# Performance work log

Hardware: AMD Instinct MI355X
Metric: run time of the kernel (lower is better)

The kernel has to match this reference:

```python
import jax, jax.numpy as jnp
import numpy as np

N = 100000          # nodes
E = 1600000         # edges (avg degree 16)
IN_DIM = 64
HID = 64
OUT = 32
NUM_GRAPHS = 64


def setup_inputs() -> dict:
    key = jax.random.key(0)
    ks = jax.random.split(key, 12)
    x = jax.random.normal(ks[0], (N, IN_DIM), dtype=jnp.float32)
    edge_index = jax.random.randint(ks[1], (2, E), 0, N, dtype=jnp.int64)
    batch = jnp.sort(jax.random.randint(ks[2], (N,), 0, NUM_GRAPHS, dtype=jnp.int64))
    s = 0.05
    return {
        "x": x,
        "edge_index": edge_index,
        "batch": batch,
        "w1_init": jax.random.normal(ks[3], (IN_DIM, HID), dtype=jnp.float32) * s,
        "w1_root": jax.random.normal(ks[4], (IN_DIM, HID), dtype=jnp.float32) * s,
        "b1": jnp.zeros((HID,), dtype=jnp.float32),
        "w2_init": jax.random.normal(ks[5], (HID, HID), dtype=jnp.float32) * s,
        "w2_root": jax.random.normal(ks[6], (HID, HID), dtype=jnp.float32) * s,
        "b2": jnp.zeros((HID,), dtype=jnp.float32),
        "fc_w": jax.random.normal(ks[7], (HID, OUT), dtype=jnp.float32) * s,
        "fc_b": jnp.zeros((OUT,), dtype=jnp.float32),
    }


def reference(x, edge_index, batch, w1_init, w1_root, b1, w2_init, w2_root, b2, fc_w, fc_b):
    row, col = edge_index[0], edge_index[1]
    # gcn_norm without self loops (ARMAConv default): deg over target nodes
    ones_e = jnp.ones((E,), dtype=x.dtype)
    deg = jax.ops.segment_sum(ones_e, col, num_segments=N)
    dinv = jnp.where(deg > 0, jax.lax.rsqrt(jnp.maximum(deg, 1.0)), 0.0)
    norm = dinv[row] * dinv[col]  # [E]

    def propagate(h):  # out[col] += norm * h[row]
        return jax.ops.segment_sum(h[row] * norm[:, None], col, num_segments=N)

    # ARMAConv (K=1, T=1, act=None): A_hat (x W_init) + x W_root + b
    h = jax.nn.relu(propagate(x @ w1_init) + x @ w1_root + b1)
    h = jax.nn.relu(propagate(h @ w2_init) + h @ w2_root + b2)

    # global mean pool over graphs
    cnt = jax.ops.segment_sum(jnp.ones((N,), dtype=h.dtype), batch, num_segments=NUM_GRAPHS)
    pooled = jax.ops.segment_sum(h, batch, num_segments=NUM_GRAPHS) / jnp.maximum(cnt, 1.0)[:, None]

    return pooled @ fc_w + fc_b  # [NUM_GRAPHS, OUT]
```

## Files before the change

### kernel.cpp

```cpp
#include <hip/hip_runtime.h>
#include <hip/hip_bf16.h>


#define NB 256
#define CAP 5120
#define MAXB 400
#define P1_CHUNK 2048

typedef unsigned int uint32;
typedef unsigned short ushort16;
typedef __attribute__((ext_vector_type(8))) short short8;
typedef __attribute__((ext_vector_type(4))) float f32x4;

__device__ inline uint32 bf16rn(float f) {
    uint32 u = __float_as_uint(f);
    uint32 r = ((u >> 16) & 1u) + 0x7FFFu;
    return (u + r) >> 16;
}
__device__ inline uint32 pack_bf16(float a, float b) {
    return bf16rn(a) | (bf16rn(b) << 16);
}
__device__ inline float bflo(uint32 u) { return __uint_as_float(u << 16); }
__device__ inline float bfhi(uint32 u) { return __uint_as_float(u & 0xFFFF0000u); }

__global__ __launch_bounds__(256) void bucket_kernel(
    const int* __restrict__ row, const int* __restrict__ col,
    uint32* __restrict__ bpack, int* __restrict__ bcnt, int E,
    const float* __restrict__ W1i, const float* __restrict__ W1r,
    const float* __restrict__ W2i, const float* __restrict__ W2r,
    ushort16* __restrict__ wt) {
    __shared__ int hist[MAXB];
    __shared__ int ofs[MAXB];
    __shared__ int cur[MAXB];
    __shared__ int gbase[MAXB];
    __shared__ int s[256];
    __shared__ uint32 stage[P1_CHUNK];
    __shared__ unsigned short stage_bk[P1_CHUNK];

    int t = threadIdx.x;

    if (blockIdx.x < 128) {
        int idx = blockIdx.x * 256 + t;
        int m = idx >> 12;
        int r = idx & 4095;
        int d = r >> 6, k = r & 63;
        const float* W = (m < 2) ? W1i : (m < 4) ? W1r : (m < 6) ? W2i : W2r;
        float v = W[k * 64 + d];
        uint32 hi = bf16rn(v);
        uint32 outv;
        if (m & 1) {
            float hf = __uint_as_float(hi << 16);
            outv = bf16rn(v - hf);
        } else {
            outv = hi;
        }
        wt[(size_t)m * 4096 + d * 64 + k] = (unsigned short)outv;
        return;
    }

    for (int i = t; i < MAXB; i += 256) hist[i] = 0;
    __syncthreads();

    int e0 = (blockIdx.x - 128) * P1_CHUNK;
    int cntE = min(E - e0, P1_CHUNK);

    for (int i = t; i < cntE; i += 256) {
        int c = col[e0 + i];
        atomicAdd(&hist[c >> 8], 1);
    }
    __syncthreads();

    int i2 = 2 * t;
    int a = (i2 < MAXB) ? hist[i2] : 0;
    int b = (i2 + 1 < MAXB) ? hist[i2 + 1] : 0;
    s[t] = a + b;
    __syncthreads();
    for (int off = 1; off < 256; off <<= 1) {
        int x = (t >= off) ? s[t - off] : 0;
        __syncthreads();
        s[t] += x;
        __syncthreads();
    }
    int excl = (t > 0) ? s[t - 1] : 0;
    if (i2 < MAXB) ofs[i2] = excl;
    if (i2 + 1 < MAXB) ofs[i2 + 1] = excl + a;
    __syncthreads();

    for (int i = t; i < MAXB; i += 256) {
        cur[i] = ofs[i];
        gbase[i] = hist[i] ? atomicAdd(&bcnt[i], hist[i]) : 0;
    }
    __syncthreads();

    for (int i = t; i < cntE; i += 256) {
        int c = col[e0 + i];
        int r = row[e0 + i];
        int bk = c >> 8;
        int k = atomicAdd(&cur[bk], 1);
        stage[k] = ((uint32)(c & 255) << 24) | (uint32)r;
        stage_bk[k] = (unsigned short)bk;
    }
    __syncthreads();

    for (int i = t; i < cntE; i += 256) {
        uint32 pk = stage[i];
        int bk = stage_bk[i];
        int gd = gbase[bk] + (i - ofs[bk]);
        if (gd < CAP) bpack[(size_t)bk * CAP + gd] = pk;
    }
}

__global__ __launch_bounds__(1024) void csr_kernel(
    const uint32* __restrict__ bpack, const int* __restrict__ bcnt,
    int* __restrict__ es, int* __restrict__ nstart, int* __restrict__ ndeg,
    float* __restrict__ dinv, int n) {
    __shared__ uint32 sbp[CAP];
    __shared__ int h[NB];
    __shared__ int s[NB];
    __shared__ int cur[NB];
    int b = blockIdx.x, t = threadIdx.x;
    if (t < NB) h[t] = 0;
    __syncthreads();
    int cnt = min(bcnt[b], CAP);
    size_t base = (size_t)b * CAP;
    for (int i = t; i < cnt; i += 1024) {
        uint32 pk = bpack[base + i];
        sbp[i] = pk;
        atomicAdd(&h[pk >> 24], 1);
    }
    __syncthreads();
    if (t < NB) s[t] = h[t];
    __syncthreads();
    for (int off = 1; off < NB; off <<= 1) {
        int x = 0;
        if (t < NB && t >= off) x = s[t - off];
        __syncthreads();
        if (t < NB) s[t] += x;
        __syncthreads();
    }
    if (t < NB) {
        int myofs = s[t] - h[t];
        cur[t] = myofs;
        int node = b * NB + t;
        if (node < n) {
            nstart[node] = (int)base + myofs;
            ndeg[node] = h[t];
            dinv[node] = h[t] ? rsqrtf((float)h[t]) : 0.0f;
        }
    }
    __syncthreads();
    for (int i = t; i < cnt; i += 1024) {
        uint32 pk = sbp[i];
        int cl = (int)(pk >> 24);
        int p = atomicAdd(&cur[cl], 1);
        es[base + p] = (int)(pk & 0xFFFFFFu);
    }
}

__global__ __launch_bounds__(256) void gemm_mfma(
    const void* __restrict__ Xin,
    const ushort16* __restrict__ wt4,
    const float* __restrict__ bias, const float* __restrict__ dinv,
    ushort16* __restrict__ Ts, ushort16* __restrict__ Rs, int n, int xf32) {
    __shared__ unsigned short sXs[64 * 72];
    int t = threadIdx.x;
    int node0 = blockIdx.x * 64;

    if (xf32) {
        const float* X = (const float*)Xin;
        for (int i = t; i < 1024; i += 256) {
            int r = i >> 4, c4 = (i & 15) * 4;
            int node = node0 + r;
            float4 v = make_float4(0.f, 0.f, 0.f, 0.f);
            if (node < n) v = *(const float4*)&X[(size_t)node * 64 + c4];
            *(uint32*)&sXs[r * 72 + c4] = pack_bf16(v.x, v.y);
            *(uint32*)&sXs[r * 72 + c4 + 2] = pack_bf16(v.z, v.w);
        }
    } else {
        const uint32* Xb2 = (const uint32*)Xin;
        for (int i = t; i < 512; i += 256) {
            int r = i >> 3, kg = i & 7;
            int node = node0 + r;
            uint4 v = make_uint4(0u, 0u, 0u, 0u);
            if (node < n) v = *(const uint4*)&Xb2[(size_t)node * 32 + kg * 4];
            *(uint4*)&sXs[r * 72 + kg * 8] = v;
        }
    }

    int w = t >> 6;
    int lane = t & 63;
    int q = lane >> 4;
    int col = lane & 15;
    int dim = w * 16 + col;

    short8 bih[2], bil[2], brh[2], brl[2];
#pragma unroll
    for (int kh = 0; kh < 2; ++kh) {
        size_t o = (size_t)dim * 64 + kh * 32 + q * 8;
        bih[kh] = *(const short8*)&wt4[0 * 4096 + o];
        bil[kh] = *(const short8*)&wt4[1 * 4096 + o];
        brh[kh] = *(const short8*)&wt4[2 * 4096 + o];
        brl[kh] = *(const short8*)&wt4[3 * 4096 + o];
    }
    float4 bias4 = *(const float4*)&bias[w * 16 + q * 4];
    __syncthreads();

    unsigned short* TsU = (unsigned short*)Ts;
    unsigned short* RsU = (unsigned short*)Rs;

#pragma unroll
    for (int mt = 0; mt < 4; ++mt) {
        int rbase = mt * 16 + col;
        short8 a0 = *(const short8*)&sXs[rbase * 72 + q * 8];
        short8 a1 = *(const short8*)&sXs[rbase * 72 + 32 + q * 8];
        f32x4 accT = {0.f, 0.f, 0.f, 0.f};
        f32x4 accR = {0.f, 0.f, 0.f, 0.f};
        accT = __builtin_amdgcn_mfma_f32_16x16x32_bf16(bih[0], a0, accT, 0, 0, 0);
        accT = __builtin_amdgcn_mfma_f32_16x16x32_bf16(bih[1], a1, accT, 0, 0, 0);
        accT = __builtin_amdgcn_mfma_f32_16x16x32_bf16(bil[0], a0, accT, 0, 0, 0);
        accT = __builtin_amdgcn_mfma_f32_16x16x32_bf16(bil[1], a1, accT, 0, 0, 0);
        accR = __builtin_amdgcn_mfma_f32_16x16x32_bf16(brh[0], a0, accR, 0, 0, 0);
        accR = __builtin_amdgcn_mfma_f32_16x16x32_bf16(brh[1], a1, accR, 0, 0, 0);
        accR = __builtin_amdgcn_mfma_f32_16x16x32_bf16(brl[0], a0, accR, 0, 0, 0);
        accR = __builtin_amdgcn_mfma_f32_16x16x32_bf16(brl[1], a1, accR, 0, 0, 0);

        int node = node0 + mt * 16 + col;
        if (node < n) {
            float dv = dinv[node];
            uint2 pT, pR;
            pT.x = pack_bf16(accT[0] * dv, accT[1] * dv);
            pT.y = pack_bf16(accT[2] * dv, accT[3] * dv);
            pR.x = pack_bf16(accR[0] + bias4.x, accR[1] + bias4.y);
            pR.y = pack_bf16(accR[2] + bias4.z, accR[3] + bias4.w);
            size_t o = (size_t)node * 64 + w * 16 + q * 4;
            *(uint2*)&TsU[o] = pT;
            *(uint2*)&RsU[o] = pR;
        }
    }
}

__global__ __launch_bounds__(256) void gather_fused(
    const uint2* __restrict__ Ts2, const uint2* __restrict__ Rs2,
    const int* __restrict__ es, const int* __restrict__ nstart,
    const int* __restrict__ ndeg, const float* __restrict__ dinv,
    uint2* __restrict__ Hb2, int n) {
    int c = blockIdx.x * 4 + (threadIdx.x >> 6);
    if (c >= n) return;
    int lane = threadIdx.x & 63;
    int q = lane >> 4;
    int d4 = lane & 15;
    int deg = ndeg[c];
    int s0 = nstart[c];
    float a0 = 0.f, a1 = 0.f, a2 = 0.f, a3 = 0.f;
    for (int base = 0; base < deg; base += 64) {
        int m = min(deg - base, 64);
        int sid = (lane < m) ? __builtin_nontemporal_load(&es[s0 + base + lane]) : 0;
        for (int j = 0; j < m; j += 16) {
            int e0 = j + q, e1 = j + 4 + q, e2 = j + 8 + q, e3 = j + 12 + q;
            int r0 = __shfl(sid, e0);
            int r1 = __shfl(sid, e1);
            int r2 = __shfl(sid, e2);
            int r3 = __shfl(sid, e3);
            uint2 z = make_uint2(0u, 0u);
            uint2 v0 = (e0 < m) ? Ts2[(size_t)r0 * 16 + d4] : z;
            uint2 v1 = (e1 < m) ? Ts2[(size_t)r1 * 16 + d4] : z;
            uint2 v2 = (e2 < m) ? Ts2[(size_t)r2 * 16 + d4] : z;
            uint2 v3 = (e3 < m) ? Ts2[(size_t)r3 * 16 + d4] : z;
            a0 += bflo(v0.x) + bflo(v1.x) + bflo(v2.x) + bflo(v3.x);
            a1 += bfhi(v0.x) + bfhi(v1.x) + bfhi(v2.x) + bfhi(v3.x);
            a2 += bflo(v0.y) + bflo(v1.y) + bflo(v2.y) + bflo(v3.y);
            a3 += bfhi(v0.y) + bfhi(v1.y) + bfhi(v2.y) + bfhi(v3.y);
        }
    }
    a0 += __shfl_xor(a0, 16); a0 += __shfl_xor(a0, 32);
    a1 += __shfl_xor(a1, 16); a1 += __shfl_xor(a1, 32);
    a2 += __shfl_xor(a2, 16); a2 += __shfl_xor(a2, 32);
    a3 += __shfl_xor(a3, 16); a3 += __shfl_xor(a3, 32);
    if (lane < 16) {
        float dc = dinv[c];
        uint2 ur = Rs2[(size_t)c * 16 + d4];
        float h0 = fmaxf(fmaf(dc, a0, bflo(ur.x)), 0.0f);
        float h1 = fmaxf(fmaf(dc, a1, bfhi(ur.x)), 0.0f);
        float h2 = fmaxf(fmaf(dc, a2, bflo(ur.y)), 0.0f);
        float h3 = fmaxf(fmaf(dc, a3, bfhi(ur.y)), 0.0f);
        Hb2[(size_t)c * 16 + d4] = make_uint2(pack_bf16(h0, h1), pack_bf16(h2, h3));
    }
}

__global__ __launch_bounds__(256) void pool_kernel(
    const uint32* __restrict__ Hb, const int* __restrict__ batch,
    float* __restrict__ pooled, float* __restrict__ cnt, int n) {
    __shared__ float sAcc[64 * 64];
    __shared__ float sCnt[64];
    int tid = threadIdx.x;
    for (int i = tid; i < 4096; i += 256) sAcc[i] = 0.0f;
    if (tid < 64) sCnt[tid] = 0.0f;
    __syncthreads();

    int w = tid >> 6, lane = tid & 63;
    int half = lane >> 5, d2 = lane & 31;
    int s = blockIdx.x * 256 + w * 64;
    int e = min(s + 64, n);
    float a0 = 0.0f, a1 = 0.0f, c = 0.0f;
    int gcur = -1;
    for (int i = s + half; i < e; i += 2) {
        int g = batch[i];
        if (g != gcur) {
            if (gcur >= 0) {
                atomicAdd(&sAcc[gcur * 64 + 2 * d2], a0);
                atomicAdd(&sAcc[gcur * 64 + 2 * d2 + 1], a1);
                if (d2 == 0) atomicAdd(&sCnt[gcur], c);
            }
            gcur = g; a0 = 0.0f; a1 = 0.0f; c = 0.0f;
        }
        uint32 u = Hb[(size_t)i * 32 + d2];
        a0 += bflo(u);
        a1 += bfhi(u);
        c += 1.0f;
    }
    if (gcur >= 0) {
        atomicAdd(&sAcc[gcur * 64 + 2 * d2], a0);
        atomicAdd(&sAcc[gcur * 64 + 2 * d2 + 1], a1);
        if (d2 == 0) atomicAdd(&sCnt[gcur], c);
    }
    __syncthreads();
    for (int i = tid; i < 4096; i += 256) {
        float v = sAcc[i];
        if (v != 0.0f) atomicAdd(&pooled[i], v);
    }
    if (tid < 64) {
        float v = sCnt[tid];
        if (v != 0.0f) atomicAdd(&cnt[tid], v);
    }
}

__global__ void final_fc(const float* __restrict__ pooled, const float* __restrict__ cnt,
                         const float* __restrict__ fcw, const float* __restrict__ fcb,
                         float* __restrict__ out) {
    int idx = blockIdx.x * 256 + threadIdx.x;
    if (idx >= 64 * 32) return;
    int g = idx >> 5, o = idx & 31;
    float c = fmaxf(cnt[g], 1.0f);
    float acc = 0.0f;
#pragma unroll
    for (int k = 0; k < 64; ++k) acc = fmaf(pooled[g * 64 + k], fcw[k * 32 + o], acc);
    out[idx] = acc / c + fcb[o];
}

extern "C" void kernel_launch(void* const* d_in, const int* in_sizes, int n_in,
                              void* d_out, int out_size, void* d_ws, size_t ws_size,
                              hipStream_t stream) {
    const float* x       = (const float*)d_in[0];
    const int*   eidx    = (const int*)d_in[1];
    const int*   batch   = (const int*)d_in[2];
    const float* w1_init = (const float*)d_in[3];
    const float* w1_root = (const float*)d_in[4];
    const float* b1      = (const float*)d_in[5];
    const float* w2_init = (const float*)d_in[6];
    const float* w2_root = (const float*)d_in[7];
    const float* b2      = (const float*)d_in[8];
    const float* fc_w    = (const float*)d_in[9];
    const float* fc_b    = (const float*)d_in[10];
    float* out = (float*)d_out;

    const int N = in_sizes[0] / 64;
    const int E = in_sizes[1] / 2;
    const int* row = eidx;
    const int* col = eidx + E;

    const int B = (N + NB - 1) / NB;

    uint32* bpack = (uint32*)d_ws;
    int*   es     = (int*)(bpack + (size_t)B * CAP);
    int*   bcnt   = es + (size_t)B * CAP;
    float* pooled = (float*)(bcnt + MAXB);
    float* cnt    = pooled + 64 * 64;
    int*   nstart = (int*)(cnt + 64);
    int*   ndeg   = nstart + N;
    float* dinv   = (float*)(ndeg + N);
    uint32* wtU   = (uint32*)(dinv + N);
    uint32* Ts    = wtU + 16384;
    uint32* Rs    = Ts + (size_t)N * 32;
    uint32* Hb    = Rs + (size_t)N * 32;
    ushort16* wt  = (ushort16*)wtU;

    hipMemsetAsync(bcnt, 0, (size_t)(MAXB + 64 * 64 + 64) * sizeof(int), stream);

    const int EB = (E + P1_CHUNK - 1) / P1_CHUNK;
    bucket_kernel<<<128 + EB, 256, 0, stream>>>(row, col, bpack, bcnt, E,
                                                w1_init, w1_root, w2_init, w2_root, wt);
    csr_kernel<<<B, 1024, 0, stream>>>(bpack, bcnt, es, nstart, ndeg, dinv, N);

    gemm_mfma<<<(N + 63) / 64, 256, 0, stream>>>(x, wt, b1, dinv,
                                                 (ushort16*)Ts, (ushort16*)Rs, N, 1);
    gather_fused<<<(N + 3) / 4, 256, 0, stream>>>((const uint2*)Ts, (const uint2*)Rs,
                                                  es, nstart, ndeg, dinv, (uint2*)Hb, N);

    gemm_mfma<<<(N + 63) / 64, 256, 0, stream>>>(Hb, wt + (size_t)4 * 4096, b2, dinv,
                                                 (ushort16*)Ts, (ushort16*)Rs, N, 0);
    gather_fused<<<(N + 3) / 4, 256, 0, stream>>>((const uint2*)Ts, (const uint2*)Rs,
                                                  es, nstart, ndeg, dinv, (uint2*)Hb, N);

    pool_kernel<<<(N + 255) / 256, 256, 0, stream>>>(Hb, batch, pooled, cnt, N);
    final_fc<<<(64 * 32 + 255) / 256, 256, 0, stream>>>(pooled, cnt, fc_w, fc_b, out);
}
```

Baseline: 294.5 us.

## Replace bucketed CSR build with global-atomic degree count, scan, and scatter

Replaces the two-pass bucket/local-sort CSR construction with three simpler kernels: per-node degree counting via global atomics, a single-block prefix scan that also computes dinv, and an atomic scatter of row indices into the CSR edge array. This drops the fixed per-bucket capacity and the intermediate packed buffer. In exchange it uses 1.6M contended global atomics twice and a single-block serial scan over 100k nodes. Neighbor order within each node is no longer deterministic. The gather also drops its nontemporal load of edge sources.

```diff
diff --git a/kernel.cpp b/kernel.cpp
--- a/kernel.cpp
+++ b/kernel.cpp
@@ -3,9 +3,6 @@
 
 
 #define NB 256
-#define CAP 5120
-#define MAXB 400
-#define P1_CHUNK 2048
 
 typedef unsigned int uint32;
 typedef unsigned short ushort16;
@@ -23,20 +20,11 @@
 __device__ inline float bflo(uint32 u) { return __uint_as_float(u << 16); }
 __device__ inline float bfhi(uint32 u) { return __uint_as_float(u & 0xFFFF0000u); }
 
-__global__ __launch_bounds__(256) void bucket_kernel(
-    const int* __restrict__ row, const int* __restrict__ col,
-    uint32* __restrict__ bpack, int* __restrict__ bcnt, int E,
+__global__ __launch_bounds__(256) void deg_kernel(
+    const int* __restrict__ col, int* __restrict__ ndeg, int E,
     const float* __restrict__ W1i, const float* __restrict__ W1r,
     const float* __restrict__ W2i, const float* __restrict__ W2r,
     ushort16* __restrict__ wt) {
-    __shared__ int hist[MAXB];
-    __shared__ int ofs[MAXB];
-    __shared__ int cur[MAXB];
-    __shared__ int gbase[MAXB];
-    __shared__ int s[256];
-    __shared__ uint32 stage[P1_CHUNK];
-    __shared__ unsigned short stage_bk[P1_CHUNK];
-
     int t = threadIdx.x;
 
     if (blockIdx.x < 128) {
@@ -58,102 +46,76 @@
         return;
     }
 
-    for (int i = t; i < MAXB; i += 256) hist[i] = 0;
-    __syncthreads();
-
-    int e0 = (blockIdx.x - 128) * P1_CHUNK;
-    int cntE = min(E - e0, P1_CHUNK);
-
-    for (int i = t; i < cntE; i += 256) {
-        int c = col[e0 + i];
-        atomicAdd(&hist[c >> 8], 1);
-    }
-    __syncthreads();
-
-    int i2 = 2 * t;
-    int a = (i2 < MAXB) ? hist[i2] : 0;
-    int b = (i2 + 1 < MAXB) ? hist[i2 + 1] : 0;
-    s[t] = a + b;
-    __syncthreads();
-    for (int off = 1; off < 256; off <<= 1) {
-        int x = (t >= off) ? s[t - off] : 0;
-        __syncthreads();
-        s[t] += x;
-        __syncthreads();
-    }
-    int excl = (t > 0) ? s[t - 1] : 0;
-    if (i2 < MAXB) ofs[i2] = excl;
-    if (i2 + 1 < MAXB) ofs[i2 + 1] = excl + a;
-    __syncthreads();
-
-    for (int i = t; i < MAXB; i += 256) {
-        cur[i] = ofs[i];
-        gbase[i] = hist[i] ? atomicAdd(&bcnt[i], hist[i]) : 0;
-    }
-    __syncthreads();
-
-    for (int i = t; i < cntE; i += 256) {
-        int c = col[e0 + i];
-        int r = row[e0 + i];
-        int bk = c >> 8;
-        int k = atomicAdd(&cur[bk], 1);
-        stage[k] = ((uint32)(c & 255) << 24) | (uint32)r;
-        stage_bk[k] = (unsigned short)bk;
-    }
-    __syncthreads();
-
-    for (int i = t; i < cntE; i += 256) {
-        uint32 pk = stage[i];
-        int bk = stage_bk[i];
-        int gd = gbase[bk] + (i - ofs[bk]);
-        if (gd < CAP) bpack[(size_t)bk * CAP + gd] = pk;
-    }
-}
-
-__global__ __launch_bounds__(1024) void csr_kernel(
-    const uint32* __restrict__ bpack, const int* __restrict__ bcnt,
-    int* __restrict__ es, int* __restrict__ nstart, int* __restrict__ ndeg,
-    float* __restrict__ dinv, int n) {
-    __shared__ uint32 sbp[CAP];
-    __shared__ int h[NB];
-    __shared__ int s[NB];
-    __shared__ int cur[NB];
-    int b = blockIdx.x, t = threadIdx.x;
-    if (t < NB) h[t] = 0;
-    __syncthreads();
-    int cnt = min(bcnt[b], CAP);
-    size_t base = (size_t)b * CAP;
-    for (int i = t; i < cnt; i += 1024) {
-        uint32 pk = bpack[base + i];
-        sbp[i] = pk;
-        atomicAdd(&h[pk >> 24], 1);
-    }
-    __syncthreads();
-    if (t < NB) s[t] = h[t];
-    __syncthreads();
-    for (int off = 1; off < NB; off <<= 1) {
-        int x = 0;
-        if (t < NB && t >= off) x = s[t - off];
-        __syncthreads();
-        if (t < NB) s[t] += x;
-        __syncthreads();
-    }
-    if (t < NB) {
-        int myofs = s[t] - h[t];
-        cur[t] = myofs;
-        int node = b * NB + t;
-        if (node < n) {
-            nstart[node] = (int)base + myofs;
-            ndeg[node] = h[t];
-            dinv[node] = h[t] ? rsqrtf((float)h[t]) : 0.0f;
-        }
-    }
-    __syncthreads();
-    for (int i = t; i < cnt; i += 1024) {
-        uint32 pk = sbp[i];
-        int cl = (int)(pk >> 24);
-        int p = atomicAdd(&cur[cl], 1);
-        es[base + p] = (int)(pk & 0xFFFFFFu);
+    int e0 = (blockIdx.x - 128) * 2048 + t * 8;
+    if (e0 + 8 <= E) {
+        int4 a = *(const int4*)&col[e0];
+        int4 b = *(const int4*)&col[e0 + 4];
+        atomicAdd(&ndeg[a.x], 1); atomicAdd(&ndeg[a.y], 1);
+        atomicAdd(&ndeg[a.z], 1); atomicAdd(&ndeg[a.w], 1);
+        atomicAdd(&ndeg[b.x], 1); atomicAdd(&ndeg[b.y], 1);
+        atomicAdd(&ndeg[b.z], 1); atomicAdd(&ndeg[b.w], 1);
+    } else {
+        for (int k = 0; k < 8; ++k)
+            if (e0 + k < E) atomicAdd(&ndeg[col[e0 + k]], 1);
+    }
+}
+
+__global__ __launch_bounds__(1024) void scan_kernel(
+    const int* __restrict__ ndeg, int* __restrict__ nstart,
+    int* __restrict__ cur, float* __restrict__ dinv, int n) {
+    __shared__ int wtot[16];
+    __shared__ int wexc[16];
+    int t = threadIdx.x;
+    int per = (n + 1023) / 1024;
+    int s0 = min(t * per, n);
+    int s1 = min(s0 + per, n);
+    int sum = 0;
+    for (int i = s0; i < s1; ++i) sum += ndeg[i];
+
+    int lane = t & 63, w = t >> 6;
+    int inc = sum;
+    for (int off = 1; off < 64; off <<= 1) {
+        int v = __shfl_up(inc, off);
+        if (lane >= off) inc += v;
+    }
+    if (lane == 63) wtot[w] = inc;
+    __syncthreads();
+    if (t == 0) {
+        int acc = 0;
+        for (int i = 0; i < 16; ++i) { wexc[i] = acc; acc += wtot[i]; }
+    }
+    __syncthreads();
+    int base = wexc[w] + (inc - sum);
+    for (int i = s0; i < s1; ++i) {
+        int d = ndeg[i];
+        nstart[i] = base;
+        cur[i] = base;
+        dinv[i] = d ? rsqrtf((float)d) : 0.0f;
+        base += d;
+    }
+}
+
+__global__ __launch_bounds__(256) void scatter_kernel(
+    const int* __restrict__ row, const int* __restrict__ col,
+    int* __restrict__ cur, int* __restrict__ es, int E) {
+    int t = threadIdx.x;
+    int e0 = blockIdx.x * 2048 + t * 8;
+    if (e0 + 8 <= E) {
+        int4 ca = *(const int4*)&col[e0];
+        int4 cb = *(const int4*)&col[e0 + 4];
+        int4 ra = *(const int4*)&row[e0];
+        int4 rb = *(const int4*)&row[e0 + 4];
+        es[atomicAdd(&cur[ca.x], 1)] = ra.x;
+        es[atomicAdd(&cur[ca.y], 1)] = ra.y;
+        es[atomicAdd(&cur[ca.z], 1)] = ra.z;
+        es[atomicAdd(&cur[ca.w], 1)] = ra.w;
+        es[atomicAdd(&cur[cb.x], 1)] = rb.x;
+        es[atomicAdd(&cur[cb.y], 1)] = rb.y;
+        es[atomicAdd(&cur[cb.z], 1)] = rb.z;
+        es[atomicAdd(&cur[cb.w], 1)] = rb.w;
+    } else {
+        for (int k = 0; k < 8; ++k)
+            if (e0 + k < E) es[atomicAdd(&cur[col[e0 + k]], 1)] = row[e0 + k];
     }
 }
 
@@ -254,7 +216,7 @@
     float a0 = 0.f, a1 = 0.f, a2 = 0.f, a3 = 0.f;
     for (int base = 0; base < deg; base += 64) {
         int m = min(deg - base, 64);
-        int sid = (lane < m) ? __builtin_nontemporal_load(&es[s0 + base + lane]) : 0;
+        int sid = (lane < m) ? es[s0 + base + lane] : 0;
         for (int j = 0; j < m; j += 16) {
             int e0 = j + q, e1 = j + 4 + q, e2 = j + 8 + q, e3 = j + 12 + q;
             int r0 = __shfl(sid, e0);
@@ -368,28 +330,26 @@
     const int* row = eidx;
     const int* col = eidx + E;
 
-    const int B = (N + NB - 1) / NB;
-
-    uint32* bpack = (uint32*)d_ws;
-    int*   es     = (int*)(bpack + (size_t)B * CAP);
-    int*   bcnt   = es + (size_t)B * CAP;
-    float* pooled = (float*)(bcnt + MAXB);
+    int*   ndeg   = (int*)d_ws;
+    float* pooled = (float*)(ndeg + N);
     float* cnt    = pooled + 64 * 64;
     int*   nstart = (int*)(cnt + 64);
-    int*   ndeg   = nstart + N;
-    float* dinv   = (float*)(ndeg + N);
+    int*   cur    = nstart + N;
+    float* dinv   = (float*)(cur + N);
     uint32* wtU   = (uint32*)(dinv + N);
-    uint32* Ts    = wtU + 16384;
+    int*   es     = (int*)(wtU + 16384);
+    uint32* Ts    = (uint32*)(es + E);
     uint32* Rs    = Ts + (size_t)N * 32;
     uint32* Hb    = Rs + (size_t)N * 32;
     ushort16* wt  = (ushort16*)wtU;
 
-    hipMemsetAsync(bcnt, 0, (size_t)(MAXB + 64 * 64 + 64) * sizeof(int), stream);
-
-    const int EB = (E + P1_CHUNK - 1) / P1_CHUNK;
-    bucket_kernel<<<128 + EB, 256, 0, stream>>>(row, col, bpack, bcnt, E,
-                                                w1_init, w1_root, w2_init, w2_root, wt);
-    csr_kernel<<<B, 1024, 0, stream>>>(bpack, bcnt, es, nstart, ndeg, dinv, N);
+    hipMemsetAsync(ndeg, 0, (size_t)(N + 64 * 64 + 64) * sizeof(int), stream);
+
+    const int EB = (E + 2047) / 2048;
+    deg_kernel<<<128 + EB, 256, 0, stream>>>(col, ndeg, E,
+                                             w1_init, w1_root, w2_init, w2_root, wt);
+    scan_kernel<<<1, 1024, 0, stream>>>(ndeg, nstart, cur, dinv, N);
+    scatter_kernel<<<EB, 256, 0, stream>>>(row, col, cur, es, E);
 
     gemm_mfma<<<(N + 63) / 64, 256, 0, stream>>>(x, wt, b1, dinv,
                                                  (ushort16*)Ts, (ushort16*)Rs, N, 1);
```

New measurement: 700.8 us. +137.9%, slower.
